# Optimization experiments

Measured on AMD Instinct MI355X. Metric: run time of the kernel, lower is better.

## Reference

```python
import jax, jax.numpy as jnp
import numpy as np


def setup_inputs() -> dict:
    key = jax.random.key(0)
    k1, k2, k3 = jax.random.split(key, 3)
    B, C, H, Wd = 32, 768, 32, 32
    K, DQ = 64, 16
    features = jax.random.normal(k1, (B, C, H, Wd), dtype=jnp.float32)
    query = jax.random.normal(k2, (B, DQ, H, Wd), dtype=jnp.float32)
    # Ensemble of 1x1 convs (bias=False): weight [K, dim_query, dim]
    W = jax.random.normal(k3, (K, DQ, C), dtype=jnp.float32) * (1.0 / np.sqrt(C))
    return {"features": features, "query": query, "W": W}


def reference(features, query, W):
    # Ensemble 1x1 conv: key_values [K, B, DQ, H, W]
    kv = jnp.einsum('bchw,kqc->kbqhw', features, W)
    K, B = kv.shape[0], kv.shape[1]
    # cdist between query (b, 1, d) and keys (b, k, d), d = DQ*H*W
    q_flat = query.reshape(B, -1)                       # [B, D]
    k_flat = jnp.moveaxis(kv.reshape(K, B, -1), 0, 1)   # [B, K, D]
    diff = q_flat[:, None, :] - k_flat                  # [B, K, D]
    distance = jnp.sqrt(jnp.sum(diff * diff, axis=-1))  # [B, K]
    # logits = -distance; codes = argmax(logits) == argmin(distance)
    codes = jnp.argmin(distance, axis=-1)               # [B]
    # per-batch gather of selected key_values
    sel = kv[codes, jnp.arange(B)]                      # [B, DQ, H, W]
    commit_loss = jnp.mean((sel - query) ** 2)
    return sel, codes, commit_loss
```

## Files before the change

kernel.cpp:

```cpp
#include <hip/hip_runtime.h>
#include <cstdint>
#include <cstddef>

typedef float f4 __attribute__((ext_vector_type(4)));
typedef float f32x4 __attribute__((ext_vector_type(4)));
typedef short short8 __attribute__((ext_vector_type(8)));
typedef unsigned short u16x8 __attribute__((ext_vector_type(8)));
typedef unsigned short u16x4 __attribute__((ext_vector_type(4)));
typedef unsigned short ushort_t;

#define B_   32
#define C_   768
#define HW_  1024
#define DQ_  16
#define K_   64
#define M_   1024
#define NHWT 16

#define CODE_OFF 524288
#define LOSS_OFF 524320

__device__ __forceinline__ unsigned bf16_rne_bits(float x) {
    unsigned u = __builtin_bit_cast(unsigned, x);
    return (u + 0x7FFFu + ((u >> 16) & 1u)) >> 16;
}
__device__ __forceinline__ float bits_to_f32(unsigned hi16) {
    unsigned u = hi16 << 16;
    return __builtin_bit_cast(float, u);
}
__device__ __forceinline__ void split_bf16(float x, unsigned short& hi, unsigned short& lo) {
    unsigned h = bf16_rne_bits(x);
    hi = (unsigned short)h;
    float r = x - bits_to_f32(h);
    lo = (unsigned short)bf16_rne_bits(r);
}

__global__ __launch_bounds__(256)
void k0_splitF(const float* __restrict__ Fp,
               ushort_t* __restrict__ FhiT, ushort_t* __restrict__ FloT)
{
    __shared__ float tile[64][65];
    const int t = threadIdx.x;
    const int ht = blockIdx.x, ct = blockIdx.y, b = blockIdx.z;

#pragma unroll
    for (int rep = 0; rep < 4; ++rep) {
        int idx = rep * 256 + t;
        int c_l = idx >> 4;
        int hwf = (idx & 15) * 4;
        f4 v = *(const f4*)&Fp[((size_t)b * C_ + ct * 64 + c_l) * HW_ + ht * 64 + hwf];
        tile[c_l][hwf + 0] = v.x;
        tile[c_l][hwf + 1] = v.y;
        tile[c_l][hwf + 2] = v.z;
        tile[c_l][hwf + 3] = v.w;
    }
    __syncthreads();

#pragma unroll
    for (int rep = 0; rep < 2; ++rep) {
        int hw_l = (t >> 3) + rep * 32;
        int cg   = (t & 7) * 8;
        unsigned short hi[8], lo[8];
#pragma unroll
        for (int j = 0; j < 8; ++j)
            split_bf16(tile[cg + j][hw_l], hi[j], lo[j]);
        size_t o = ((size_t)b * HW_ + ht * 64 + hw_l) * C_ + ct * 64 + cg;
        *(u16x8*)&FhiT[o] = *(u16x8*)hi;
        *(u16x8*)&FloT[o] = *(u16x8*)lo;
    }
}

__global__ __launch_bounds__(256)
void k0_splitW(const float* __restrict__ Wp,
               ushort_t* __restrict__ Whi, ushort_t* __restrict__ Wlo)
{
    size_t base = ((size_t)blockIdx.x * 256 + threadIdx.x) * 4;
    f4 v = *(const f4*)&Wp[base];
    unsigned short hi[4], lo[4];
    split_bf16(v.x, hi[0], lo[0]);
    split_bf16(v.y, hi[1], lo[1]);
    split_bf16(v.z, hi[2], lo[2]);
    split_bf16(v.w, hi[3], lo[3]);
    *(u16x4*)&Whi[base] = *(u16x4*)hi;
    *(u16x4*)&Wlo[base] = *(u16x4*)lo;
}

#define NKT 36

__global__ __launch_bounds__(512, 2)
void k1_mfma8(const ushort_t* __restrict__ Whi, const ushort_t* __restrict__ Wlo,
              const ushort_t* __restrict__ FhiT, const ushort_t* __restrict__ FloT,
              const float* __restrict__ Qp, float* __restrict__ partial)
{
    __shared__ ushort_t lds[2][32768];

    const int tid  = threadIdx.x;
    const int w    = tid >> 6;
    const int lane = tid & 63;

    const int bid = blockIdx.x;
    const int idx = (bid & 7) * 64 + (bid >> 3);
    const int mt  = idx & 3;
    const int hwt = (idx >> 2) & 3;
    const int b   = idx >> 4;

    const int wm = w >> 2, wn = w & 3;

    const bool isA    = (w < 4);
    const int  wrow0  = (w & 3) * 64;
    const int  srow   = lane >> 3;
    const int  sslot  = (lane & 7) ^ srow;
    const int  regoff = isA ? 0 : 16384;
    const size_t abase = (size_t)(mt * 256) * C_;
    const size_t bbase = ((size_t)b * HW_ + hwt * 256) * C_;

    const int c15 = lane & 15, d0 = lane >> 4;
    int offA[8][2], offB[4][2];
#pragma unroll
    for (int i = 0; i < 8; ++i) {
        int m = wm * 128 + i * 16 + c15;
#pragma unroll
        for (int kh = 0; kh < 2; ++kh) {
            int d = kh * 4 + d0;
            offA[i][kh] = m * 64 + ((d ^ (m & 7)) << 3);
        }
    }
#pragma unroll
    for (int j = 0; j < 4; ++j) {
        int n = wn * 64 + j * 16 + c15;
#pragma unroll
        for (int kh = 0; kh < 2; ++kh) {
            int d = kh * 4 + d0;
            offB[j][kh] = 16384 + n * 64 + ((d ^ (n & 7)) << 3);
        }
    }

    f32x4 acc[8][4] = {};

    {
        const ushort_t* sb = isA ? (Whi + abase) : (FhiT + bbase);
#pragma unroll
        for (int ii = 0; ii < 8; ++ii) {
            const ushort_t* g = sb + (size_t)(wrow0 + ii * 8 + srow) * C_ + sslot * 8;
            __builtin_amdgcn_global_load_lds(
                (const __attribute__((address_space(1))) void*)g,
                (__attribute__((address_space(3))) void*)&lds[0][regoff + (wrow0 + ii * 8) * 64],
                16, 0, 0);
        }
    }
    asm volatile("s_waitcnt vmcnt(0)" ::: "memory");
    __builtin_amdgcn_s_barrier();

    short8 af[4][2], bf0[2][2], bf1[2][2];

#define STAGE2(II)                                                                              \
    if (do_stage) {                                                                             \
        const ushort_t* g0 = sb + (size_t)(wrow0 + (II) * 8 + srow) * C_ + sslot * 8;           \
        __builtin_amdgcn_global_load_lds(                                                       \
            (const __attribute__((address_space(1))) void*)g0,                                  \
            (__attribute__((address_space(3))) void*)(Lnext + regoff + (wrow0 + (II) * 8) * 64),\
            16, 0, 0);                                                                          \
        const ushort_t* g1 = sb + (size_t)(wrow0 + (II) * 8 + 8 + srow) * C_ + sslot * 8;       \
        __builtin_amdgcn_global_load_lds(                                                       \
            (const __attribute__((address_space(1))) void*)g1,                                  \
            (__attribute__((address_space(3))) void*)(Lnext + regoff + (wrow0 + (II) * 8 + 8) * 64),\
            16, 0, 0);                                                                          \
    }

#define QUAD(I0, J0, BF)                                                                        \
    _Pragma("unroll")                                                                           \
    for (int i4 = 0; i4 < 4; ++i4)                                                              \
        _Pragma("unroll")                                                                       \
        for (int j2 = 0; j2 < 2; ++j2)                                                          \
            _Pragma("unroll")                                                                   \
            for (int kh = 0; kh < 2; ++kh)                                                      \
                acc[(I0) + i4][(J0) + j2] = __builtin_amdgcn_mfma_f32_16x16x32_bf16(            \
                    af[i4][kh], BF[j2][kh], acc[(I0) + i4][(J0) + j2], 0, 0, 0);

#define PRE_MFMA()                                          \
    __builtin_amdgcn_s_barrier();                           \
    asm volatile("s_waitcnt lgkmcnt(0)" ::: "memory");      \
    __builtin_amdgcn_sched_barrier(0);                      \
    __builtin_amdgcn_s_setprio(1);

#define POST_MFMA()                                         \
    __builtin_amdgcn_s_setprio(0);                          \
    __builtin_amdgcn_sched_barrier(0);                      \
    __builtin_amdgcn_s_barrier();

    for (int t = 0; t < NKT; ++t) {
        const int cur = t & 1;
        const ushort_t* L = &lds[cur][0];
        ushort_t* Lnext = &lds[cur ^ 1][0];

        const bool do_stage = (t + 1 < NKT);
        const int tt = do_stage ? (t + 1) : 0;
        const int term = (tt >= 24) ? 2 : ((tt >= 12) ? 1 : 0);
        const int c0 = (tt - term * 12) * 64;
        const ushort_t* sb;
        if (isA) sb = ((term == 1) ? Wlo : Whi) + abase + c0;
        else     sb = ((term == 2) ? FloT : FhiT) + bbase + c0;

#pragma unroll
        for (int i4 = 0; i4 < 4; ++i4)
#pragma unroll
            for (int kh = 0; kh < 2; ++kh)
                af[i4][kh] = *(const short8*)&L[offA[i4][kh]];
#pragma unroll
        for (int j2 = 0; j2 < 2; ++j2)
#pragma unroll
            for (int kh = 0; kh < 2; ++kh)
                bf0[j2][kh] = *(const short8*)&L[offB[j2][kh]];
        STAGE2(0)
        PRE_MFMA()
        QUAD(0, 0, bf0)
        POST_MFMA()

#pragma unroll
        for (int j2 = 0; j2 < 2; ++j2)
#pragma unroll
            for (int kh = 0; kh < 2; ++kh)
                bf1[j2][kh] = *(const short8*)&L[offB[2 + j2][kh]];
        STAGE2(2)
        PRE_MFMA()
        QUAD(0, 2, bf1)
        POST_MFMA()

#pragma unroll
        for (int i4 = 0; i4 < 4; ++i4)
#pragma unroll
            for (int kh = 0; kh < 2; ++kh)
                af[i4][kh] = *(const short8*)&L[offA[4 + i4][kh]];
        STAGE2(4)
        PRE_MFMA()
        QUAD(4, 2, bf1)
        POST_MFMA()

        STAGE2(6)
        __builtin_amdgcn_s_barrier();
        __builtin_amdgcn_sched_barrier(0);
        __builtin_amdgcn_s_setprio(1);
        QUAD(4, 0, bf0)
        __builtin_amdgcn_s_setprio(0);
        __builtin_amdgcn_sched_barrier(0);
        asm volatile("s_waitcnt vmcnt(0)" ::: "memory");
        __builtin_amdgcn_s_barrier();
    }
#undef STAGE2
#undef QUAD
#undef PRE_MFMA
#undef POST_MFMA

    float qv[4][4];
#pragma unroll
    for (int j = 0; j < 4; ++j) {
        const int hw = hwt * 256 + wn * 64 + j * 16 + c15;
#pragma unroll
        for (int r = 0; r < 4; ++r)
            qv[j][r] = Qp[(size_t)(b * DQ_ + d0 * 4 + r) * HW_ + hw];
    }
#pragma unroll
    for (int i = 0; i < 8; ++i) {
        float s = 0.f;
#pragma unroll
        for (int j = 0; j < 4; ++j)
#pragma unroll
            for (int r = 0; r < 4; ++r) {
                float d = qv[j][r] - acc[i][j][r];
                s = fmaf(d, d, s);
            }
#pragma unroll
        for (int off = 32; off; off >>= 1) s += __shfl_xor(s, off);
        if (lane == 0) {
            const int k = mt * 16 + wm * 8 + i;
            partial[((size_t)b * K_ + k) * NHWT + hwt * 4 + wn] = s;
        }
    }
}

#define BM   256
#define BN   64
#define BC   32
#define NMT  4

__global__ __launch_bounds__(256)
void k1_dist_fp32(const float* __restrict__ Fp, const float* __restrict__ Qp,
                  const float* __restrict__ Wp, float* __restrict__ partial)
{
    __shared__ float w_lds[BC][BM];
    __shared__ float f_lds[BC][BN + 8];
    __shared__ float red[32][8];

    const int tid = threadIdx.x;
    const int mt = blockIdx.x, hwt = blockIdx.y, b = blockIdx.z;
    const int ty = tid >> 3, tx = tid & 7;
    const int m0 = ty * 8, hw0 = tx * 8;

    float acc[8][8];
#pragma unroll
    for (int i = 0; i < 8; ++i)
#pragma unroll
        for (int j = 0; j < 8; ++j) acc[i][j] = 0.f;

    for (int c0 = 0; c0 < C_; c0 += BC) {
#pragma unroll
        for (int i = 0; i < 8; ++i) {
            const int m_l = i * 32 + ty;
            const int c_l = tx * 4;
            const int col = m_l ^ (tx * 4);
            f4 w4 = *(const f4*)&Wp[(size_t)(mt * BM + m_l) * C_ + c0 + c_l];
            w_lds[c_l + 0][col] = w4.x;
            w_lds[c_l + 1][col] = w4.y;
            w_lds[c_l + 2][col] = w4.z;
            w_lds[c_l + 3][col] = w4.w;
        }
        {
            const int c = tid >> 3;
            const int hw = (tid & 7) * 8;
            const float* src = &Fp[((size_t)b * C_ + c0 + c) * HW_ + (size_t)hwt * BN + hw];
            *(f4*)&f_lds[c][hw]     = *(const f4*)src;
            *(f4*)&f_lds[c][hw + 4] = *(const f4*)(src + 4);
        }
        __syncthreads();

#pragma unroll 4
        for (int cc = 0; cc < BC; ++cc) {
            const int sw = ((cc >> 2) & 7) * 4;
            const int colA = m0 ^ sw;
            f4 w0 = *(const f4*)&w_lds[cc][colA];
            f4 w1 = *(const f4*)&w_lds[cc][colA ^ 4];
            f4 g0 = *(const f4*)&f_lds[cc][hw0];
            f4 g1 = *(const f4*)&f_lds[cc][hw0 + 4];
            const float wa[8] = {w0.x, w0.y, w0.z, w0.w, w1.x, w1.y, w1.z, w1.w};
            const float fv[8] = {g0.x, g0.y, g0.z, g0.w, g1.x, g1.y, g1.z, g1.w};
#pragma unroll
            for (int i = 0; i < 8; ++i)
#pragma unroll
                for (int j = 0; j < 8; ++j)
                    acc[i][j] = fmaf(wa[i], fv[j], acc[i][j]);
        }
        __syncthreads();
    }

    const int q0 = (ty & 1) * 8;
    float s = 0.f;
#pragma unroll
    for (int i = 0; i < 8; ++i) {
        const float* qp = &Qp[((size_t)b * DQ_ + q0 + i) * HW_ + (size_t)hwt * BN + hw0];
        f4 qa = *(const f4*)qp;
        f4 qb = *(const f4*)(qp + 4);
        float d;
        d = qa.x - acc[i][0]; s = fmaf(d, d, s);
        d = qa.y - acc[i][1]; s = fmaf(d, d, s);
        d = qa.z - acc[i][2]; s = fmaf(d, d, s);
        d = qa.w - acc[i][3]; s = fmaf(d, d, s);
        d = qb.x - acc[i][4]; s = fmaf(d, d, s);
        d = qb.y - acc[i][5]; s = fmaf(d, d, s);
        d = qb.z - acc[i][6]; s = fmaf(d, d, s);
        d = qb.w - acc[i][7]; s = fmaf(d, d, s);
    }
    red[ty][tx] = s;
    __syncthreads();
    if (tid < 16) {
        float t = 0.f;
#pragma unroll
        for (int r = 0; r < 2; ++r)
#pragma unroll
            for (int x = 0; x < 8; ++x) t += red[tid * 2 + r][x];
        partial[((size_t)b * K_ + mt * 16 + tid) * NHWT + hwt] = t;
    }
}

__global__ __launch_bounds__(1024)
void k2_select(const float* __restrict__ partial, float* __restrict__ out,
               int* __restrict__ codes_ws)
{
    const int tid = threadIdx.x;
    const int b = tid >> 5, kk = tid & 31;
    float s0 = 0.f, s1 = 0.f;
#pragma unroll
    for (int h = 0; h < NHWT; ++h) {
        s0 += partial[((size_t)b * K_ + kk) * NHWT + h];
        s1 += partial[((size_t)b * K_ + kk + 32) * NHWT + h];
    }
    float bv = s0; int bk = kk;
    if (s1 < bv) { bv = s1; bk = kk + 32; }
#pragma unroll
    for (int m = 16; m >= 1; m >>= 1) {
        float ov = __shfl_xor(bv, m);
        int   ok = __shfl_xor(bk, m);
        if (ov < bv || (ov == bv && ok < bk)) { bv = ov; bk = ok; }
    }
    __shared__ float mins[32];
    if (kk == 0) {
        out[CODE_OFF + b] = (float)bk;
        codes_ws[b] = bk;
        mins[b] = bv;
    }
    __syncthreads();
    if (tid == 0) {
        float t = 0.f;
#pragma unroll
        for (int i = 0; i < 32; ++i) t += mins[i];
        out[LOSS_OFF] = t * (1.0f / 524288.0f);
    }
}

#define BN3 128
#define BC3 32

__global__ __launch_bounds__(256)
void k3_sel(const float* __restrict__ Fp, const float* __restrict__ Wp,
            const int* __restrict__ codes_ws, float* __restrict__ out)
{
    __shared__ float f_lds[BC3][BN3];
    __shared__ float w_lds[DQ_][33];

    const int tid = threadIdx.x;
    const int b = blockIdx.x >> 3, hwt = blockIdx.x & 7;
    const int code = codes_ws[b];
    const int q = tid >> 4;
    const int hw0 = (tid & 15) * 8;

    float a[8] = {0.f, 0.f, 0.f, 0.f, 0.f, 0.f, 0.f, 0.f};

    for (int c0 = 0; c0 < C_; c0 += BC3) {
        if (tid < 128) {
            const int qq = tid >> 3, c4 = (tid & 7) * 4;
            f4 w4 = *(const f4*)&Wp[((size_t)code * DQ_ + qq) * C_ + c0 + c4];
            w_lds[qq][c4 + 0] = w4.x;
            w_lds[qq][c4 + 1] = w4.y;
            w_lds[qq][c4 + 2] = w4.z;
            w_lds[qq][c4 + 3] = w4.w;
        }
        {
            const int c = tid >> 3;
            const int hw = (tid & 7) * 16;
            const float* src = &Fp[((size_t)b * C_ + c0 + c) * HW_ + (size_t)hwt * BN3 + hw];
            *(f4*)&f_lds[c][hw]      = *(const f4*)(src);
            *(f4*)&f_lds[c][hw + 4]  = *(const f4*)(src + 4);
            *(f4*)&f_lds[c][hw + 8]  = *(const f4*)(src + 8);
            *(f4*)&f_lds[c][hw + 12] = *(const f4*)(src + 12);
        }
        __syncthreads();
#pragma unroll 4
        for (int cc = 0; cc < BC3; ++cc) {
            const float wv = w_lds[q][cc];
            f4 g0 = *(const f4*)&f_lds[cc][hw0];
            f4 g1 = *(const f4*)&f_lds[cc][hw0 + 4];
            a[0] = fmaf(wv, g0.x, a[0]);
            a[1] = fmaf(wv, g0.y, a[1]);
            a[2] = fmaf(wv, g0.z, a[2]);
            a[3] = fmaf(wv, g0.w, a[3]);
            a[4] = fmaf(wv, g1.x, a[4]);
            a[5] = fmaf(wv, g1.y, a[5]);
            a[6] = fmaf(wv, g1.z, a[6]);
            a[7] = fmaf(wv, g1.w, a[7]);
        }
        __syncthreads();
    }

    float* dst = &out[((size_t)b * DQ_ + q) * HW_ + (size_t)hwt * BN3 + hw0];
    f4 o0 = {a[0], a[1], a[2], a[3]};
    f4 o1 = {a[4], a[5], a[6], a[7]};
    *(f4*)dst = o0;
    *(f4*)(dst + 4) = o1;
}

extern "C" void kernel_launch(void* const* d_in, const int* in_sizes, int n_in,
                              void* d_out, int out_size, void* d_ws, size_t ws_size,
                              hipStream_t stream)
{
    const float* Fp = (const float*)d_in[0];
    const float* Qp = (const float*)d_in[1];
    const float* Wp = (const float*)d_in[2];
    float* out = (float*)d_out;

    const size_t FT_ELEMS = (size_t)B_ * HW_ * C_;
    const size_t W_ELEMS  = (size_t)M_ * C_;
    const size_t PART_OFF = 4 * FT_ELEMS + 4 * W_ELEMS;
    const size_t CODE_WS  = PART_OFF + (size_t)B_ * K_ * NHWT * 4;
    const size_t NEED     = CODE_WS + 128;

    if (ws_size >= NEED) {
        ushort_t* FhiT = (ushort_t*)d_ws;
        ushort_t* FloT = FhiT + FT_ELEMS;
        ushort_t* Whi  = FloT + FT_ELEMS;
        ushort_t* Wlo  = Whi + W_ELEMS;
        float* partial = (float*)((char*)d_ws + PART_OFF);
        int* codes_ws  = (int*)((char*)d_ws + CODE_WS);

        k0_splitF<<<dim3(16, 12, B_), 256, 0, stream>>>(Fp, FhiT, FloT);
        k0_splitW<<<dim3(W_ELEMS / 1024), 256, 0, stream>>>(Wp, Whi, Wlo);
        k1_mfma8<<<dim3(512), 512, 0, stream>>>(Whi, Wlo, FhiT, FloT, Qp, partial);
        k2_select<<<1, 1024, 0, stream>>>(partial, out, codes_ws);
        k3_sel<<<dim3(B_ * 8), 256, 0, stream>>>(Fp, Wp, codes_ws, out);
    } else {
        float* partial = (float*)d_ws;
        int* codes_ws  = (int*)((char*)d_ws + (size_t)B_ * K_ * NHWT * 4);
        k1_dist_fp32<<<dim3(NMT, NHWT, B_), 256, 0, stream>>>(Fp, Qp, Wp, partial);
        k2_select<<<1, 1024, 0, stream>>>(partial, out, codes_ws);
        k3_sel<<<dim3(B_ * 8), 256, 0, stream>>>(Fp, Wp, codes_ws, out);
    }
}
```

Measured before the change: 349.9 us.

## Tile split bf16 buffers by channel block and compute selection with MFMA

Stores the hi/lo bf16 copies of F and W in channel-tiled [ct][rows][64] layouts so each K-step of the main MFMA kernel reads one contiguous block instead of strided rows. Staging is regrouped into two batches of four loads per stage instead of four batches of two. The final selected-key-value kernel is replaced by an MFMA kernel that reuses the split bf16 buffers (three-term hi/lo product) instead of re-reading fp32 features. This trades fp32 exactness in the gather step for the 3xbf16 approximation and reshapes the staging schedule.

```diff
diff --git a/kernel.cpp b/kernel.cpp
--- a/kernel.cpp
+++ b/kernel.cpp
@@ -16,6 +16,7 @@
 #define K_   64
 #define M_   1024
 #define NHWT 16
+#define NCT  12
 
 #define CODE_OFF 524288
 #define LOSS_OFF 524320
@@ -34,6 +35,7 @@
     float r = x - bits_to_f32(h);
     lo = (unsigned short)bf16_rne_bits(r);
 }
+
 
 __global__ __launch_bounds__(256)
 void k0_splitF(const float* __restrict__ Fp,
@@ -64,7 +66,7 @@
 #pragma unroll
         for (int j = 0; j < 8; ++j)
             split_bf16(tile[cg + j][hw_l], hi[j], lo[j]);
-        size_t o = ((size_t)b * HW_ + ht * 64 + hw_l) * C_ + ct * 64 + cg;
+        size_t o = (((size_t)(b * NCT + ct)) * HW_ + ht * 64 + hw_l) * 64 + cg;
         *(u16x8*)&FhiT[o] = *(u16x8*)hi;
         *(u16x8*)&FloT[o] = *(u16x8*)lo;
     }
@@ -74,15 +76,20 @@
 void k0_splitW(const float* __restrict__ Wp,
                ushort_t* __restrict__ Whi, ushort_t* __restrict__ Wlo)
 {
-    size_t base = ((size_t)blockIdx.x * 256 + threadIdx.x) * 4;
+    const unsigned gid = blockIdx.x * 256 + threadIdx.x;
+    const unsigned base = gid * 4;
+    const unsigned m = base / C_;
+    const unsigned c = base - m * C_;
+    const unsigned ct = c >> 6, cl = c & 63;
     f4 v = *(const f4*)&Wp[base];
     unsigned short hi[4], lo[4];
     split_bf16(v.x, hi[0], lo[0]);
     split_bf16(v.y, hi[1], lo[1]);
     split_bf16(v.z, hi[2], lo[2]);
     split_bf16(v.w, hi[3], lo[3]);
-    *(u16x4*)&Whi[base] = *(u16x4*)hi;
-    *(u16x4*)&Wlo[base] = *(u16x4*)lo;
+    size_t o = ((size_t)ct * M_ + m) * 64 + cl;
+    *(u16x4*)&Whi[o] = *(u16x4*)hi;
+    *(u16x4*)&Wlo[o] = *(u16x4*)lo;
 }
 
 #define NKT 36
@@ -111,8 +118,6 @@
     const int  srow   = lane >> 3;
     const int  sslot  = (lane & 7) ^ srow;
     const int  regoff = isA ? 0 : 16384;
-    const size_t abase = (size_t)(mt * 256) * C_;
-    const size_t bbase = ((size_t)b * HW_ + hwt * 256) * C_;
 
     const int c15 = lane & 15, d0 = lane >> 4;
     int offA[8][2], offB[4][2];
@@ -138,10 +143,11 @@
     f32x4 acc[8][4] = {};
 
     {
-        const ushort_t* sb = isA ? (Whi + abase) : (FhiT + bbase);
+        const ushort_t* sb = isA ? (Whi + (size_t)(mt * 256) * 64)
+                                 : (FhiT + ((size_t)(b * NCT) * HW_ + hwt * 256) * 64);
 #pragma unroll
         for (int ii = 0; ii < 8; ++ii) {
-            const ushort_t* g = sb + (size_t)(wrow0 + ii * 8 + srow) * C_ + sslot * 8;
+            const ushort_t* g = sb + (size_t)(wrow0 + ii * 8 + srow) * 64 + sslot * 8;
             __builtin_amdgcn_global_load_lds(
                 (const __attribute__((address_space(1))) void*)g,
                 (__attribute__((address_space(3))) void*)&lds[0][regoff + (wrow0 + ii * 8) * 64],
@@ -153,28 +159,26 @@
 
     short8 af[4][2], bf0[2][2], bf1[2][2];
 
-#define STAGE2(II)                                                                              \
-    if (do_stage) {                                                                             \
-        const ushort_t* g0 = sb + (size_t)(wrow0 + (II) * 8 + srow) * C_ + sslot * 8;           \
-        __builtin_amdgcn_global_load_lds(                                                       \
-            (const __attribute__((address_space(1))) void*)g0,                                  \
-            (__attribute__((address_space(3))) void*)(Lnext + regoff + (wrow0 + (II) * 8) * 64),\
-            16, 0, 0);                                                                          \
-        const ushort_t* g1 = sb + (size_t)(wrow0 + (II) * 8 + 8 + srow) * C_ + sslot * 8;       \
-        __builtin_amdgcn_global_load_lds(                                                       \
-            (const __attribute__((address_space(1))) void*)g1,                                  \
-            (__attribute__((address_space(3))) void*)(Lnext + regoff + (wrow0 + (II) * 8 + 8) * 64),\
-            16, 0, 0);                                                                          \
-    }
-
-#define QUAD(I0, J0, BF)                                                                        \
-    _Pragma("unroll")                                                                           \
-    for (int i4 = 0; i4 < 4; ++i4)                                                              \
-        _Pragma("unroll")                                                                       \
-        for (int j2 = 0; j2 < 2; ++j2)                                                          \
-            _Pragma("unroll")                                                                   \
-            for (int kh = 0; kh < 2; ++kh)                                                      \
-                acc[(I0) + i4][(J0) + j2] = __builtin_amdgcn_mfma_f32_16x16x32_bf16(            \
+#define STAGE4(II)                                                                               \
+    if (do_stage) {                                                                              \
+        _Pragma("unroll")                                                                        \
+        for (int ii = (II); ii < (II) + 4; ++ii) {                                               \
+            const ushort_t* g = sb + (size_t)(wrow0 + ii * 8 + srow) * 64 + sslot * 8;           \
+            __builtin_amdgcn_global_load_lds(                                                    \
+                (const __attribute__((address_space(1))) void*)g,                                \
+                (__attribute__((address_space(3))) void*)(Lnext + regoff + (wrow0 + ii * 8) * 64),\
+                16, 0, 0);                                                                       \
+        }                                                                                        \
+    }
+
+#define QUAD(I0, J0, BF)                                                                         \
+    _Pragma("unroll")                                                                            \
+    for (int i4 = 0; i4 < 4; ++i4)                                                               \
+        _Pragma("unroll")                                                                        \
+        for (int j2 = 0; j2 < 2; ++j2)                                                           \
+            _Pragma("unroll")                                                                    \
+            for (int kh = 0; kh < 2; ++kh)                                                       \
+                acc[(I0) + i4][(J0) + j2] = __builtin_amdgcn_mfma_f32_16x16x32_bf16(             \
                     af[i4][kh], BF[j2][kh], acc[(I0) + i4][(J0) + j2], 0, 0, 0);
 
 #define PRE_MFMA()                                          \
@@ -196,10 +200,10 @@
         const bool do_stage = (t + 1 < NKT);
         const int tt = do_stage ? (t + 1) : 0;
         const int term = (tt >= 24) ? 2 : ((tt >= 12) ? 1 : 0);
-        const int c0 = (tt - term * 12) * 64;
+        const int ct = tt - term * 12;
         const ushort_t* sb;
-        if (isA) sb = ((term == 1) ? Wlo : Whi) + abase + c0;
-        else     sb = ((term == 2) ? FloT : FhiT) + bbase + c0;
+        if (isA) sb = ((term == 1) ? Wlo : Whi) + ((size_t)ct * M_ + mt * 256) * 64;
+        else     sb = ((term == 2) ? FloT : FhiT) + ((size_t)(b * NCT + ct) * HW_ + hwt * 256) * 64;
 
 #pragma unroll
         for (int i4 = 0; i4 < 4; ++i4)
@@ -211,7 +215,7 @@
 #pragma unroll
             for (int kh = 0; kh < 2; ++kh)
                 bf0[j2][kh] = *(const short8*)&L[offB[j2][kh]];
-        STAGE2(0)
+        STAGE4(0)
         PRE_MFMA()
         QUAD(0, 0, bf0)
         POST_MFMA()
@@ -221,7 +225,7 @@
 #pragma unroll
             for (int kh = 0; kh < 2; ++kh)
                 bf1[j2][kh] = *(const short8*)&L[offB[2 + j2][kh]];
-        STAGE2(2)
+        STAGE4(4)
         PRE_MFMA()
         QUAD(0, 2, bf1)
         POST_MFMA()
@@ -231,12 +235,10 @@
 #pragma unroll
             for (int kh = 0; kh < 2; ++kh)
                 af[i4][kh] = *(const short8*)&L[offA[4 + i4][kh]];
-        STAGE2(4)
         PRE_MFMA()
         QUAD(4, 2, bf1)
         POST_MFMA()
 
-        STAGE2(6)
         __builtin_amdgcn_s_barrier();
         __builtin_amdgcn_sched_barrier(0);
         __builtin_amdgcn_s_setprio(1);
@@ -246,7 +248,7 @@
         asm volatile("s_waitcnt vmcnt(0)" ::: "memory");
         __builtin_amdgcn_s_barrier();
     }
-#undef STAGE2
+#undef STAGE4
 #undef QUAD
 #undef PRE_MFMA
 #undef POST_MFMA
@@ -275,6 +277,140 @@
             const int k = mt * 16 + wm * 8 + i;
             partial[((size_t)b * K_ + k) * NHWT + hwt * 4 + wn] = s;
         }
+    }
+}
+
+__global__ __launch_bounds__(1024)
+void k2_select(const float* __restrict__ partial, float* __restrict__ out,
+               int* __restrict__ codes_ws)
+{
+    const int tid = threadIdx.x;
+    const int b = tid >> 5, kk = tid & 31;
+    float s0 = 0.f, s1 = 0.f;
+#pragma unroll
+    for (int h = 0; h < NHWT; ++h) {
+        s0 += partial[((size_t)b * K_ + kk) * NHWT + h];
+        s1 += partial[((size_t)b * K_ + kk + 32) * NHWT + h];
+    }
+    float bv = s0; int bk = kk;
+    if (s1 < bv) { bv = s1; bk = kk + 32; }
+#pragma unroll
+    for (int m = 16; m >= 1; m >>= 1) {
+        float ov = __shfl_xor(bv, m);
+        int   ok = __shfl_xor(bk, m);
+        if (ov < bv || (ov == bv && ok < bk)) { bv = ov; bk = ok; }
+    }
+    __shared__ float mins[32];
+    if (kk == 0) {
+        out[CODE_OFF + b] = (float)bk;
+        codes_ws[b] = bk;
+        mins[b] = bv;
+    }
+    __syncthreads();
+    if (tid == 0) {
+        float t = 0.f;
+#pragma unroll
+        for (int i = 0; i < 32; ++i) t += mins[i];
+        out[LOSS_OFF] = t * (1.0f / 524288.0f);
+    }
+}
+
+__global__ __launch_bounds__(256)
+void k3_mfma(const ushort_t* __restrict__ Whi, const ushort_t* __restrict__ Wlo,
+             const ushort_t* __restrict__ FhiT, const ushort_t* __restrict__ FloT,
+             const int* __restrict__ codes_ws, float* __restrict__ out)
+{
+    __shared__ ushort_t lds3[2][10240];
+
+    const int tid = threadIdx.x;
+    const int w = tid >> 6, lane = tid & 63;
+    const int b = blockIdx.x >> 4, hwt = blockIdx.x & 15;
+    const int code = codes_ws[b];
+
+    const int srow = lane >> 3, sslot = (lane & 7) ^ srow;
+    const int c15 = lane & 15, d0 = lane >> 4;
+
+    int offAhi[2], offAlo[2], offBh[2], offBl[2];
+#pragma unroll
+    for (int kh = 0; kh < 2; ++kh) {
+        const int d = kh * 4 + d0;
+        const int mA = c15;
+        offAhi[kh] = mA * 64 + ((d ^ (mA & 7)) << 3);
+        const int mAl = 16 + c15;
+        offAlo[kh] = mAl * 64 + ((d ^ (mAl & 7)) << 3);
+        const int rB = w * 16 + c15;
+        offBh[kh] = 2048 + rB * 64 + ((d ^ (rB & 7)) << 3);
+        offBl[kh] = 6144 + rB * 64 + ((d ^ (rB & 7)) << 3);
+    }
+
+#define K3_STAGE(CT, BUF)                                                                        \
+    {                                                                                            \
+        ushort_t* Lb = &lds3[(BUF)][0];                                                          \
+        const ushort_t* bhp = FhiT + ((size_t)(b * NCT + (CT)) * HW_ + hwt * 64) * 64;           \
+        const ushort_t* blp = FloT + ((size_t)(b * NCT + (CT)) * HW_ + hwt * 64) * 64;           \
+        _Pragma("unroll")                                                                        \
+        for (int ii = 0; ii < 2; ++ii) {                                                         \
+            __builtin_amdgcn_global_load_lds(                                                    \
+                (const __attribute__((address_space(1))) void*)(bhp + (w * 16 + ii * 8 + srow) * 64 + sslot * 8), \
+                (__attribute__((address_space(3))) void*)(Lb + 2048 + (w * 16 + ii * 8) * 64),   \
+                16, 0, 0);                                                                       \
+            __builtin_amdgcn_global_load_lds(                                                    \
+                (const __attribute__((address_space(1))) void*)(blp + (w * 16 + ii * 8 + srow) * 64 + sslot * 8), \
+                (__attribute__((address_space(3))) void*)(Lb + 6144 + (w * 16 + ii * 8) * 64),   \
+                16, 0, 0);                                                                       \
+        }                                                                                        \
+        if (w == 0) {                                                                            \
+            const ushort_t* ahp = Whi + ((size_t)(CT) * M_ + code * 16) * 64;                    \
+            _Pragma("unroll")                                                                    \
+            for (int ii = 0; ii < 2; ++ii)                                                       \
+                __builtin_amdgcn_global_load_lds(                                                \
+                    (const __attribute__((address_space(1))) void*)(ahp + (ii * 8 + srow) * 64 + sslot * 8), \
+                    (__attribute__((address_space(3))) void*)(Lb + (ii * 8) * 64),               \
+                    16, 0, 0);                                                                   \
+        } else if (w == 1) {                                                                     \
+            const ushort_t* alp = Wlo + ((size_t)(CT) * M_ + code * 16) * 64;                    \
+            _Pragma("unroll")                                                                    \
+            for (int ii = 0; ii < 2; ++ii)                                                       \
+                __builtin_amdgcn_global_load_lds(                                                \
+                    (const __attribute__((address_space(1))) void*)(alp + (ii * 8 + srow) * 64 + sslot * 8), \
+                    (__attribute__((address_space(3))) void*)(Lb + (16 + ii * 8) * 64),          \
+                    16, 0, 0);                                                                   \
+        }                                                                                        \
+    }
+
+    f32x4 acc = {};
+
+    K3_STAGE(0, 0)
+    asm volatile("s_waitcnt vmcnt(0)" ::: "memory");
+    __syncthreads();
+
+    for (int ct = 0; ct < NCT; ++ct) {
+        const int cur = ct & 1;
+        if (ct + 1 < NCT) K3_STAGE(ct + 1, cur ^ 1)
+        const ushort_t* L = &lds3[cur][0];
+        short8 ah[2], al2[2], bh[2], bl[2];
+#pragma unroll
+        for (int kh = 0; kh < 2; ++kh) {
+            ah[kh]  = *(const short8*)&L[offAhi[kh]];
+            al2[kh] = *(const short8*)&L[offAlo[kh]];
+            bh[kh]  = *(const short8*)&L[offBh[kh]];
+            bl[kh]  = *(const short8*)&L[offBl[kh]];
+        }
+#pragma unroll
+        for (int kh = 0; kh < 2; ++kh) {
+            acc = __builtin_amdgcn_mfma_f32_16x16x32_bf16(ah[kh], bh[kh], acc, 0, 0, 0);
+            acc = __builtin_amdgcn_mfma_f32_16x16x32_bf16(ah[kh], bl[kh], acc, 0, 0, 0);
+            acc = __builtin_amdgcn_mfma_f32_16x16x32_bf16(al2[kh], bh[kh], acc, 0, 0, 0);
+        }
+        asm volatile("s_waitcnt vmcnt(0)" ::: "memory");
+        __syncthreads();
+    }
+#undef K3_STAGE
+
+#pragma unroll
+    for (int r = 0; r < 4; ++r) {
+        const int q = d0 * 4 + r;
+        out[((size_t)(b * DQ_ + q)) * HW_ + hwt * 64 + w * 16 + c15] = acc[r];
     }
 }
 
@@ -368,41 +504,6 @@
 #pragma unroll
             for (int x = 0; x < 8; ++x) t += red[tid * 2 + r][x];
         partial[((size_t)b * K_ + mt * 16 + tid) * NHWT + hwt] = t;
-    }
-}
-
-__global__ __launch_bounds__(1024)
-void k2_select(const float* __restrict__ partial, float* __restrict__ out,
-               int* __restrict__ codes_ws)
-{
-    const int tid = threadIdx.x;
-    const int b = tid >> 5, kk = tid & 31;
-    float s0 = 0.f, s1 = 0.f;
-#pragma unroll
-    for (int h = 0; h < NHWT; ++h) {
-        s0 += partial[((size_t)b * K_ + kk) * NHWT + h];
-        s1 += partial[((size_t)b * K_ + kk + 32) * NHWT + h];
-    }
-    float bv = s0; int bk = kk;
-    if (s1 < bv) { bv = s1; bk = kk + 32; }
-#pragma unroll
-    for (int m = 16; m >= 1; m >>= 1) {
-        float ov = __shfl_xor(bv, m);
-        int   ok = __shfl_xor(bk, m);
-        if (ov < bv || (ov == bv && ok < bk)) { bv = ov; bk = ok; }
-    }
-    __shared__ float mins[32];
-    if (kk == 0) {
-        out[CODE_OFF + b] = (float)bk;
-        codes_ws[b] = bk;
-        mins[b] = bv;
-    }
-    __syncthreads();
-    if (tid == 0) {
-        float t = 0.f;
-#pragma unroll
-        for (int i = 0; i < 32; ++i) t += mins[i];
-        out[LOSS_OFF] = t * (1.0f / 524288.0f);
     }
 }
 
@@ -490,11 +591,11 @@
         float* partial = (float*)((char*)d_ws + PART_OFF);
         int* codes_ws  = (int*)((char*)d_ws + CODE_WS);
 
-        k0_splitF<<<dim3(16, 12, B_), 256, 0, stream>>>(Fp, FhiT, FloT);
+        k0_splitF<<<dim3(16, NCT, B_), 256, 0, stream>>>(Fp, FhiT, FloT);
         k0_splitW<<<dim3(W_ELEMS / 1024), 256, 0, stream>>>(Wp, Whi, Wlo);
         k1_mfma8<<<dim3(512), 512, 0, stream>>>(Whi, Wlo, FhiT, FloT, Qp, partial);
         k2_select<<<1, 1024, 0, stream>>>(partial, out, codes_ws);
-        k3_sel<<<dim3(B_ * 8), 256, 0, stream>>>(Fp, Wp, codes_ws, out);
+        k3_mfma<<<dim3(B_ * 16), 256, 0, stream>>>(Whi, Wlo, FhiT, FloT, codes_ws, out);
     } else {
         float* partial = (float*)d_ws;
         int* codes_ws  = (int*)((char*)d_ws + (size_t)B_ * K_ * NHWT * 4);
```

Result: faster. 309.6 us (-11.5%).
